# Performance work log

Measured on AMD Instinct MI355X. Metric: run time of the kernel, lower is better.

Reference implementation:

```python
import jax, jax.numpy as jnp
import numpy as np

EPS = 1e-6      # torch F.pairwise_distance default eps (added to the difference)
MARGIN = 1.0

def _cdist_eps(a, b):
    # Exact ||a_i - b_j + eps||_2 via expansion:
    # ||a-b+eps||^2 = ||a||^2 + ||b||^2 - 2 a.b + 2*eps*(sum(a)-sum(b)) + D*eps^2
    D = a.shape[-1]
    sq = (jnp.sum(a * a, axis=1)[:, None]
          + jnp.sum(b * b, axis=1)[None, :]
          - 2.0 * (a @ b.T)
          + 2.0 * EPS * (jnp.sum(a, axis=1)[:, None] - jnp.sum(b, axis=1)[None, :])
          + D * EPS * EPS)
    return jnp.sqrt(jnp.maximum(sq, 0.0))

def setup_inputs() -> dict:
    key = jax.random.key(0)
    k1, k2, k3 = jax.random.split(key, 3)
    B, D = 4096, 1024
    return {
        'anchor_embeddings': jax.random.normal(k1, (B, D), dtype=jnp.float32),
        'positive_embeddings': jax.random.normal(k2, (B, D), dtype=jnp.float32),
        'negative_embeddings': jax.random.normal(k3, (B, D), dtype=jnp.float32),
    }

def reference(anchor_embeddings, positive_embeddings, negative_embeddings):
    a, p, n = anchor_embeddings, positive_embeddings, negative_embeddings
    # per-row anchor-positive and anchor-negative distances
    d_ap = jnp.linalg.norm(a - p + EPS, axis=-1)          # [B]
    d_an_row = jnp.linalg.norm(a - n + EPS, axis=-1)      # [B]

    # hardest negative: for each anchor, max over negatives with dist < d_ap[i], else 0
    dan_mat = _cdist_eps(a, n)                            # [B, B]
    mask_n = dan_mat < d_ap[:, None]
    hard_n = jnp.where(mask_n.any(axis=1),
                       jnp.max(jnp.where(mask_n, dan_mat, -jnp.inf), axis=1),
                       0.0)
    d_an = jnp.mean(hard_n)                               # scalar

    # hardest positive: for each anchor, min over positives with dist > d(a_i, n_i), else 0
    dpp_mat = _cdist_eps(a, p)                            # [B, B]
    mask_p = dpp_mat > d_an_row[:, None]
    hard_p = jnp.where(mask_p.any(axis=1),
                       jnp.min(jnp.where(mask_p, dpp_mat, jnp.inf), axis=1),
                       0.0)
    d_pp = jnp.mean(hard_p)                               # scalar

    loss = jnp.mean(jnp.clip(d_ap - 0.5 * d_pp - 0.5 * d_an + MARGIN, 0.0, None))
    return loss
```

## Files before the change

kernel.cpp:

```cpp
#include <hip/hip_runtime.h>


#define NB 4096
#define DIM 1024
#define EPSF 1e-6f
#define D_EPS2 (1024.0f * 1e-6f * 1e-6f)

#define BM 128
#define BK 32

typedef __bf16  bf16x8 __attribute__((ext_vector_type(8)));
typedef float   f32x4  __attribute__((ext_vector_type(4)));

__device__ __forceinline__ unsigned short f2bf(float x) {
    unsigned u = __float_as_uint(x);
    u += 0x7FFFu + ((u >> 16) & 1u);
    return (unsigned short)(u >> 16);
}

__device__ __forceinline__ void g2l16(const unsigned short* g, unsigned short* l) {
    __builtin_amdgcn_global_load_lds(
        (const __attribute__((address_space(1))) unsigned int*)g,
        (__attribute__((address_space(3))) unsigned int*)l, 16, 0, 0);
}


__global__ __launch_bounds__(256) void row_stats_kernel(
    const float* __restrict__ a, const float* __restrict__ p,
    const float* __restrict__ n,
    unsigned short* __restrict__ abf, unsigned short* __restrict__ pbf,
    unsigned short* __restrict__ nbf, float* __restrict__ stats)
{
    const int row = blockIdx.x;
    const int t   = threadIdx.x;
    const size_t base = (size_t)row * DIM;

    float4 va = ((const float4*)(a + base))[t];
    float4 vp = ((const float4*)(p + base))[t];
    float4 vn = ((const float4*)(n + base))[t];

    float v[8] = {0,0,0,0,0,0,0,0};
    const float fa[4] = {va.x, va.y, va.z, va.w};
    const float fp[4] = {vp.x, vp.y, vp.z, vp.w};
    const float fn[4] = {vn.x, vn.y, vn.z, vn.w};
#pragma unroll
    for (int e = 0; e < 4; e++) {
        v[0] += fa[e];           v[1] += fa[e] * fa[e];
        v[2] += fp[e];           v[3] += fp[e] * fp[e];
        v[4] += fn[e];           v[5] += fn[e] * fn[e];
        float dp = fa[e] - fp[e] + EPSF;  v[6] += dp * dp;
        float dn = fa[e] - fn[e] + EPSF;  v[7] += dn * dn;
    }

    ushort4 ba, bp, bn;
    ba.x = f2bf(fa[0]); ba.y = f2bf(fa[1]); ba.z = f2bf(fa[2]); ba.w = f2bf(fa[3]);
    bp.x = f2bf(fp[0]); bp.y = f2bf(fp[1]); bp.z = f2bf(fp[2]); bp.w = f2bf(fp[3]);
    bn.x = f2bf(fn[0]); bn.y = f2bf(fn[1]); bn.z = f2bf(fn[2]); bn.w = f2bf(fn[3]);
    ((ushort4*)(abf + base))[t] = ba;
    ((ushort4*)(pbf + base))[t] = bp;
    ((ushort4*)(nbf + base))[t] = bn;

#pragma unroll
    for (int m = 32; m >= 1; m >>= 1)
#pragma unroll
        for (int q = 0; q < 8; q++) v[q] += __shfl_xor(v[q], m);

    __shared__ float part[4][8];
    const int wave = t >> 6, lane = t & 63;
    if (lane == 0)
#pragma unroll
        for (int q = 0; q < 8; q++) part[wave][q] = v[q];
    __syncthreads();
    if (t == 0) {
        float r[8];
#pragma unroll
        for (int q = 0; q < 8; q++)
            r[q] = part[0][q] + part[1][q] + part[2][q] + part[3][q];
        stats[0 * NB + row] = r[0];
        stats[1 * NB + row] = r[1];
        stats[2 * NB + row] = r[2];
        stats[3 * NB + row] = r[3];
        stats[4 * NB + row] = r[4];
        stats[5 * NB + row] = r[5];
        stats[6 * NB + row] = sqrtf(r[6]);
        stats[7 * NB + row] = sqrtf(r[7]);
        ((unsigned*)stats)[8 * NB + row] = 0u;
        ((unsigned*)stats)[9 * NB + row] = 0x7f800000u;
    }
}

__global__ __launch_bounds__(256, 2) void gemm_mask_kernel(
    const unsigned short* __restrict__ Abf,
    const unsigned short* __restrict__ Nbf,
    const unsigned short* __restrict__ Pbf,
    float* __restrict__ stats)
{
    const int i0 = blockIdx.x * BM;
    const int j0 = blockIdx.y * BM;
    const bool isP = (blockIdx.z != 0);
    const unsigned short* __restrict__ Bmat = isP ? Pbf : Nbf;

    __shared__ unsigned short sA[BM * BK];
    __shared__ unsigned short sB[BM * BK];

    const int t    = threadIdx.x;
    const int wave = t >> 6, lane = t & 63;
    const int wm   = wave >> 1, wn = wave & 1;
    const int quad = lane >> 4, lrow = lane & 15;

    const int lrow4 = lane >> 2;
    const int kch   = ((lane & 3) ^ ((lane >> 3) & 3)) * 8;
    const unsigned short* ga0 = Abf  + (size_t)(i0 + wave * 32 + lrow4) * DIM + kch;
    const unsigned short* ga1 = ga0 + 16 * DIM;
    const unsigned short* gb0 = Bmat + (size_t)(j0 + wave * 32 + lrow4) * DIM + kch;
    const unsigned short* gb1 = gb0 + 16 * DIM;
    unsigned short* la0 = sA + (wave * 32) * BK;
    unsigned short* la1 = la0 + 16 * BK;
    unsigned short* lb0 = sB + (wave * 32) * BK;
    unsigned short* lb1 = lb0 + 16 * BK;

    const int rsw = (quad ^ ((lrow >> 1) & 3)) * 8;
    const unsigned short* pa = sA + (wm * 64 + lrow) * BK + rsw;
    const unsigned short* pb = sB + (wn * 64 + lrow) * BK + rsw;

    f32x4 acc[4][4];
#pragma unroll
    for (int im = 0; im < 4; im++)
#pragma unroll
        for (int jn = 0; jn < 4; jn++) acc[im][jn] = (f32x4)(0.0f);

    for (int kt = 0; kt < DIM; kt += BK) {
        __syncthreads();
        g2l16(ga0, la0);
        g2l16(ga1, la1);
        g2l16(gb0, lb0);
        g2l16(gb1, lb1);
        ga0 += BK; ga1 += BK; gb0 += BK; gb1 += BK;
        __syncthreads();

        bf16x8 afr[4], bfr[4];
#pragma unroll
        for (int im = 0; im < 4; im++)
            afr[im] = *(const bf16x8*)(pa + im * 16 * BK);
#pragma unroll
        for (int jn = 0; jn < 4; jn++)
            bfr[jn] = *(const bf16x8*)(pb + jn * 16 * BK);
#pragma unroll
        for (int im = 0; im < 4; im++)
#pragma unroll
            for (int jn = 0; jn < 4; jn++)
                acc[im][jn] = __builtin_amdgcn_mfma_f32_16x16x32_bf16(
                    afr[im], bfr[jn], acc[im][jn], 0, 0, 0);
    }

    const float* __restrict__ sum_a = stats + 0 * NB;
    const float* __restrict__ nrm_a = stats + 1 * NB;
    const float* __restrict__ sum_b = isP ? (stats + 2 * NB) : (stats + 4 * NB);
    const float* __restrict__ nrm_b = isP ? (stats + 3 * NB) : (stats + 5 * NB);
    const float* __restrict__ cut_v = isP ? (stats + 7 * NB) : (stats + 6 * NB);
    unsigned* __restrict__ hard = ((unsigned*)stats) + (isP ? 9 : 8) * NB;

#pragma unroll
    for (int im = 0; im < 4; im++) {
#pragma unroll
        for (int r = 0; r < 4; r++) {
            const int gi = i0 + wm * 64 + im * 16 + quad * 4 + r;
            const float cut    = cut_v[gi];
            const float base_i = nrm_a[gi] + 2.0f * EPSF * sum_a[gi] + D_EPS2;
            float best = isP ? __uint_as_float(0x7f800000u) : 0.0f;
#pragma unroll
            for (int jn = 0; jn < 4; jn++) {
                const int gj = j0 + wn * 64 + jn * 16 + lrow;
                const float c  = acc[im][jn][r];
                const float sq = base_i + nrm_b[gj] - 2.0f * c - 2.0f * EPSF * sum_b[gj];
                const float dist = sqrtf(fmaxf(sq, 0.0f));
                if (isP) { if (dist > cut && dist < best) best = dist; }
                else     { if (dist < cut && dist > best) best = dist; }
            }
#pragma unroll
            for (int m = 1; m < 16; m <<= 1) {
                float o = __shfl_xor(best, m);
                best = isP ? fminf(best, o) : fmaxf(best, o);
            }
            if (lrow == 0) {
                const unsigned bits = __float_as_uint(best);
                if (isP) { if (bits != 0x7f800000u) atomicMin(hard + gi, bits); }
                else     { if (bits != 0u)          atomicMax(hard + gi, bits); }
            }
        }
    }
}

__global__ __launch_bounds__(256) void finalize_kernel(
    const float* __restrict__ stats, float* __restrict__ out)
{
    const unsigned* hard_n = ((const unsigned*)stats) + 8 * NB;
    const unsigned* hard_p = ((const unsigned*)stats) + 9 * NB;
    const float*    d_ap   = stats + 6 * NB;
    const int t = threadIdx.x;
    const int wave = t >> 6, lane = t & 63;
    __shared__ float pn[4], pp[4];
    __shared__ float s_dan, s_dpp;

    float sn = 0.0f, sp = 0.0f;
    for (int i = t; i < NB; i += 256) {
        sn += __uint_as_float(hard_n[i]);
        const unsigned hp = hard_p[i];
        if (hp != 0x7f800000u) sp += __uint_as_float(hp);
    }
#pragma unroll
    for (int m = 32; m >= 1; m >>= 1) {
        sn += __shfl_xor(sn, m);
        sp += __shfl_xor(sp, m);
    }
    if (lane == 0) { pn[wave] = sn; pp[wave] = sp; }
    __syncthreads();
    if (t == 0) {
        s_dan = (pn[0] + pn[1] + pn[2] + pn[3]) / (float)NB;
        s_dpp = (pp[0] + pp[1] + pp[2] + pp[3]) / (float)NB;
    }
    __syncthreads();
    const float dan = s_dan, dpp = s_dpp;

    float accv = 0.0f;
    for (int i = t; i < NB; i += 256)
        accv += fmaxf(d_ap[i] - 0.5f * dpp - 0.5f * dan + 1.0f, 0.0f);
#pragma unroll
    for (int m = 32; m >= 1; m >>= 1) accv += __shfl_xor(accv, m);
    if (lane == 0) pn[wave] = accv;
    __syncthreads();
    if (t == 0) out[0] = (pn[0] + pn[1] + pn[2] + pn[3]) / (float)NB;
}

extern "C" void kernel_launch(void* const* d_in, const int* in_sizes, int n_in,
                              void* d_out, int out_size, void* d_ws, size_t ws_size,
                              hipStream_t stream) {
    const float* a = (const float*)d_in[0];
    const float* p = (const float*)d_in[1];
    const float* n = (const float*)d_in[2];
    float* out = (float*)d_out;

    unsigned short* abf = (unsigned short*)d_ws;
    unsigned short* pbf = abf + (size_t)NB * DIM;
    unsigned short* nbf = pbf + (size_t)NB * DIM;
    float* stats = (float*)(nbf + (size_t)NB * DIM);

    row_stats_kernel<<<NB, 256, 0, stream>>>(a, p, n, abf, pbf, nbf, stats);

    dim3 grid(NB / BM, NB / BM, 2);
    gemm_mask_kernel<<<grid, 256, 0, stream>>>(abf, nbf, pbf, stats);

    finalize_kernel<<<1, 256, 0, stream>>>(stats, out);
}
```

Before: 217.5 us.

## Fuse negative and positive distance GEMMs sharing anchor tile in one kernel

Merges the two z-slices of the masked distance GEMM into a single block that loads the anchor tile once and computes both anchor-negative and anchor-positive accumulators. Row-stat constants are precomputed into combined bias terms so the epilogue does fewer loads and flops. The finalize kernel is widened to 1024 threads. Doubles accumulator registers per thread, risking lower occupancy or spills.

```diff
diff --git a/kernel.cpp b/kernel.cpp
--- a/kernel.cpp
+++ b/kernel.cpp
@@ -76,16 +76,13 @@
 #pragma unroll
         for (int q = 0; q < 8; q++)
             r[q] = part[0][q] + part[1][q] + part[2][q] + part[3][q];
-        stats[0 * NB + row] = r[0];
-        stats[1 * NB + row] = r[1];
-        stats[2 * NB + row] = r[2];
-        stats[3 * NB + row] = r[3];
-        stats[4 * NB + row] = r[4];
-        stats[5 * NB + row] = r[5];
-        stats[6 * NB + row] = sqrtf(r[6]);
-        stats[7 * NB + row] = sqrtf(r[7]);
-        ((unsigned*)stats)[8 * NB + row] = 0u;
-        ((unsigned*)stats)[9 * NB + row] = 0x7f800000u;
+        stats[0 * NB + row] = r[1] + 2.0f * EPSF * r[0] + D_EPS2;
+        stats[1 * NB + row] = r[5] - 2.0f * EPSF * r[4];
+        stats[2 * NB + row] = r[3] - 2.0f * EPSF * r[2];
+        stats[3 * NB + row] = sqrtf(r[6]);
+        stats[4 * NB + row] = sqrtf(r[7]);
+        ((unsigned*)stats)[5 * NB + row] = 0u;
+        ((unsigned*)stats)[6 * NB + row] = 0x7f800000u;
     }
 }
 
@@ -97,11 +94,10 @@
 {
     const int i0 = blockIdx.x * BM;
     const int j0 = blockIdx.y * BM;
-    const bool isP = (blockIdx.z != 0);
-    const unsigned short* __restrict__ Bmat = isP ? Pbf : Nbf;
 
     __shared__ unsigned short sA[BM * BK];
-    __shared__ unsigned short sB[BM * BK];
+    __shared__ unsigned short sN[BM * BK];
+    __shared__ unsigned short sP[BM * BK];
 
     const int t    = threadIdx.x;
     const int wave = t >> 6, lane = t & 63;
@@ -110,100 +106,113 @@
 
     const int lrow4 = lane >> 2;
     const int kch   = ((lane & 3) ^ ((lane >> 3) & 3)) * 8;
-    const unsigned short* ga0 = Abf  + (size_t)(i0 + wave * 32 + lrow4) * DIM + kch;
+    const size_t grow = (size_t)(wave * 32 + lrow4);
+    const unsigned short* ga0 = Abf + (size_t)(i0) * DIM + grow * DIM + kch;
+    const unsigned short* gn0 = Nbf + (size_t)(j0) * DIM + grow * DIM + kch;
+    const unsigned short* gp0 = Pbf + (size_t)(j0) * DIM + grow * DIM + kch;
     const unsigned short* ga1 = ga0 + 16 * DIM;
-    const unsigned short* gb0 = Bmat + (size_t)(j0 + wave * 32 + lrow4) * DIM + kch;
-    const unsigned short* gb1 = gb0 + 16 * DIM;
-    unsigned short* la0 = sA + (wave * 32) * BK;
-    unsigned short* la1 = la0 + 16 * BK;
-    unsigned short* lb0 = sB + (wave * 32) * BK;
-    unsigned short* lb1 = lb0 + 16 * BK;
+    const unsigned short* gn1 = gn0 + 16 * DIM;
+    const unsigned short* gp1 = gp0 + 16 * DIM;
+    unsigned short* la0 = sA + (wave * 32) * BK;  unsigned short* la1 = la0 + 16 * BK;
+    unsigned short* ln0 = sN + (wave * 32) * BK;  unsigned short* ln1 = ln0 + 16 * BK;
+    unsigned short* lp0 = sP + (wave * 32) * BK;  unsigned short* lp1 = lp0 + 16 * BK;
 
     const int rsw = (quad ^ ((lrow >> 1) & 3)) * 8;
-    const unsigned short* pa = sA + (wm * 64 + lrow) * BK + rsw;
-    const unsigned short* pb = sB + (wn * 64 + lrow) * BK + rsw;
-
-    f32x4 acc[4][4];
+    const unsigned short* pa  = sA + (wm * 64 + lrow) * BK + rsw;
+    const unsigned short* pbn = sN + (wn * 64 + lrow) * BK + rsw;
+    const unsigned short* pbp = sP + (wn * 64 + lrow) * BK + rsw;
+
+    f32x4 accN[4][4], accP[4][4];
 #pragma unroll
     for (int im = 0; im < 4; im++)
 #pragma unroll
-        for (int jn = 0; jn < 4; jn++) acc[im][jn] = (f32x4)(0.0f);
+        for (int jn = 0; jn < 4; jn++) {
+            accN[im][jn] = (f32x4)(0.0f);
+            accP[im][jn] = (f32x4)(0.0f);
+        }
 
     for (int kt = 0; kt < DIM; kt += BK) {
         __syncthreads();
-        g2l16(ga0, la0);
-        g2l16(ga1, la1);
-        g2l16(gb0, lb0);
-        g2l16(gb1, lb1);
-        ga0 += BK; ga1 += BK; gb0 += BK; gb1 += BK;
+        g2l16(ga0, la0);  g2l16(ga1, la1);
+        g2l16(gn0, ln0);  g2l16(gn1, ln1);
+        g2l16(gp0, lp0);  g2l16(gp1, lp1);
+        ga0 += BK; ga1 += BK; gn0 += BK; gn1 += BK; gp0 += BK; gp1 += BK;
         __syncthreads();
 
-        bf16x8 afr[4], bfr[4];
+        bf16x8 afr[4], bn_fr[4], bp_fr[4];
 #pragma unroll
         for (int im = 0; im < 4; im++)
             afr[im] = *(const bf16x8*)(pa + im * 16 * BK);
 #pragma unroll
-        for (int jn = 0; jn < 4; jn++)
-            bfr[jn] = *(const bf16x8*)(pb + jn * 16 * BK);
+        for (int jn = 0; jn < 4; jn++) {
+            bn_fr[jn] = *(const bf16x8*)(pbn + jn * 16 * BK);
+            bp_fr[jn] = *(const bf16x8*)(pbp + jn * 16 * BK);
+        }
 #pragma unroll
         for (int im = 0; im < 4; im++)
 #pragma unroll
-            for (int jn = 0; jn < 4; jn++)
-                acc[im][jn] = __builtin_amdgcn_mfma_f32_16x16x32_bf16(
-                    afr[im], bfr[jn], acc[im][jn], 0, 0, 0);
-    }
-
-    const float* __restrict__ sum_a = stats + 0 * NB;
-    const float* __restrict__ nrm_a = stats + 1 * NB;
-    const float* __restrict__ sum_b = isP ? (stats + 2 * NB) : (stats + 4 * NB);
-    const float* __restrict__ nrm_b = isP ? (stats + 3 * NB) : (stats + 5 * NB);
-    const float* __restrict__ cut_v = isP ? (stats + 7 * NB) : (stats + 6 * NB);
-    unsigned* __restrict__ hard = ((unsigned*)stats) + (isP ? 9 : 8) * NB;
+            for (int jn = 0; jn < 4; jn++) {
+                accN[im][jn] = __builtin_amdgcn_mfma_f32_16x16x32_bf16(
+                    afr[im], bn_fr[jn], accN[im][jn], 0, 0, 0);
+                accP[im][jn] = __builtin_amdgcn_mfma_f32_16x16x32_bf16(
+                    afr[im], bp_fr[jn], accP[im][jn], 0, 0, 0);
+            }
+    }
+
+    const float* __restrict__ base_a = stats + 0 * NB;
+    const float* __restrict__ cn_v   = stats + 1 * NB;
+    const float* __restrict__ cp_v   = stats + 2 * NB;
+    const float* __restrict__ d_ap   = stats + 3 * NB;
+    const float* __restrict__ d_an   = stats + 4 * NB;
+    unsigned* __restrict__ hard_n = ((unsigned*)stats) + 5 * NB;
+    unsigned* __restrict__ hard_p = ((unsigned*)stats) + 6 * NB;
 
 #pragma unroll
     for (int im = 0; im < 4; im++) {
 #pragma unroll
         for (int r = 0; r < 4; r++) {
             const int gi = i0 + wm * 64 + im * 16 + quad * 4 + r;
-            const float cut    = cut_v[gi];
-            const float base_i = nrm_a[gi] + 2.0f * EPSF * sum_a[gi] + D_EPS2;
-            float best = isP ? __uint_as_float(0x7f800000u) : 0.0f;
+            const float cutN = d_ap[gi];
+            const float cutP = d_an[gi];
+            const float bi   = base_a[gi];
+            float bestN = 0.0f;
+            float bestP = __uint_as_float(0x7f800000u);
 #pragma unroll
             for (int jn = 0; jn < 4; jn++) {
                 const int gj = j0 + wn * 64 + jn * 16 + lrow;
-                const float c  = acc[im][jn][r];
-                const float sq = base_i + nrm_b[gj] - 2.0f * c - 2.0f * EPSF * sum_b[gj];
-                const float dist = sqrtf(fmaxf(sq, 0.0f));
-                if (isP) { if (dist > cut && dist < best) best = dist; }
-                else     { if (dist < cut && dist > best) best = dist; }
+                const float dN = sqrtf(fmaxf(bi + cn_v[gj] - 2.0f * accN[im][jn][r], 0.0f));
+                const float dP = sqrtf(fmaxf(bi + cp_v[gj] - 2.0f * accP[im][jn][r], 0.0f));
+                if (dN < cutN && dN > bestN) bestN = dN;
+                if (dP > cutP && dP < bestP) bestP = dP;
             }
 #pragma unroll
             for (int m = 1; m < 16; m <<= 1) {
-                float o = __shfl_xor(best, m);
-                best = isP ? fminf(best, o) : fmaxf(best, o);
+                bestN = fmaxf(bestN, __shfl_xor(bestN, m));
+                bestP = fminf(bestP, __shfl_xor(bestP, m));
             }
             if (lrow == 0) {
-                const unsigned bits = __float_as_uint(best);
-                if (isP) { if (bits != 0x7f800000u) atomicMin(hard + gi, bits); }
-                else     { if (bits != 0u)          atomicMax(hard + gi, bits); }
+                const unsigned bn_ = __float_as_uint(bestN);
+                const unsigned bp_ = __float_as_uint(bestP);
+                if (bn_ != 0u)          atomicMax(hard_n + gi, bn_);
+                if (bp_ != 0x7f800000u) atomicMin(hard_p + gi, bp_);
             }
         }
     }
 }
 
-__global__ __launch_bounds__(256) void finalize_kernel(
+__global__ __launch_bounds__(1024) void finalize_kernel(
     const float* __restrict__ stats, float* __restrict__ out)
 {
-    const unsigned* hard_n = ((const unsigned*)stats) + 8 * NB;
-    const unsigned* hard_p = ((const unsigned*)stats) + 9 * NB;
-    const float*    d_ap   = stats + 6 * NB;
+    const unsigned* hard_n = ((const unsigned*)stats) + 5 * NB;
+    const unsigned* hard_p = ((const unsigned*)stats) + 6 * NB;
+    const float*    d_ap   = stats + 3 * NB;
     const int t = threadIdx.x;
     const int wave = t >> 6, lane = t & 63;
-    __shared__ float pn[4], pp[4];
+    __shared__ float pn[16], pp[16];
     __shared__ float s_dan, s_dpp;
 
     float sn = 0.0f, sp = 0.0f;
-    for (int i = t; i < NB; i += 256) {
+    for (int i = t; i < NB; i += 1024) {
         sn += __uint_as_float(hard_n[i]);
         const unsigned hp = hard_p[i];
         if (hp != 0x7f800000u) sp += __uint_as_float(hp);
@@ -216,20 +225,28 @@
     if (lane == 0) { pn[wave] = sn; pp[wave] = sp; }
     __syncthreads();
     if (t == 0) {
-        s_dan = (pn[0] + pn[1] + pn[2] + pn[3]) / (float)NB;
-        s_dpp = (pp[0] + pp[1] + pp[2] + pp[3]) / (float)NB;
+        float an = 0.0f, ap = 0.0f;
+#pragma unroll
+        for (int w = 0; w < 16; w++) { an += pn[w]; ap += pp[w]; }
+        s_dan = an / (float)NB;
+        s_dpp = ap / (float)NB;
     }
     __syncthreads();
     const float dan = s_dan, dpp = s_dpp;
 
     float accv = 0.0f;
-    for (int i = t; i < NB; i += 256)
+    for (int i = t; i < NB; i += 1024)
         accv += fmaxf(d_ap[i] - 0.5f * dpp - 0.5f * dan + 1.0f, 0.0f);
 #pragma unroll
     for (int m = 32; m >= 1; m >>= 1) accv += __shfl_xor(accv, m);
     if (lane == 0) pn[wave] = accv;
     __syncthreads();
-    if (t == 0) out[0] = (pn[0] + pn[1] + pn[2] + pn[3]) / (float)NB;
+    if (t == 0) {
+        float s = 0.0f;
+#pragma unroll
+        for (int w = 0; w < 16; w++) s += pn[w];
+        out[0] = s / (float)NB;
+    }
 }
 
 extern "C" void kernel_launch(void* const* d_in, const int* in_sizes, int n_in,
@@ -247,8 +264,8 @@
 
     row_stats_kernel<<<NB, 256, 0, stream>>>(a, p, n, abf, pbf, nbf, stats);
 
-    dim3 grid(NB / BM, NB / BM, 2);
+    dim3 grid(NB / BM, NB / BM);
     gemm_mask_kernel<<<grid, 256, 0, stream>>>(abf, nbf, pbf, stats);
 
-    finalize_kernel<<<1, 256, 0, stream>>>(stats, out);
-}
+    finalize_kernel<<<1, 1024, 0, stream>>>(stats, out);
+}
```

After: 195.2 us. 1.11x faster.
